# Performance work log

Hardware: AMD Instinct MI355X
Metric: run time of the kernel (lower is better)

The kernel has to match this reference:

```python
import jax, jax.numpy as jnp
import numpy as np
import math

D = 128      # out_dim (= d)
H = 4        # n_heads
DK = D // H  # d_k = 32
M = 5        # fixed num types in forward
NN = 15      # fixed N in forward
SQRT_DK = math.sqrt(DK)


def setup_inputs() -> dict:
    key = jax.random.key(0)
    ks = jax.random.split(key, 18)
    b, n = 1024, 64
    inp = {
        "node_inp": jax.random.normal(ks[0], (D, b, n), jnp.float32),
        "WW": jax.random.normal(ks[1], (b, M, n, NN), jnp.float32) * 0.1,
        "mask_matrix": jax.random.uniform(ks[2], (M * NN, n), jnp.float32),
        "R": jax.random.normal(ks[3], (b, H, n, n), jnp.float32),
        "attn_mask": jax.random.uniform(ks[4], (1, 1, n, 4 * n), jnp.float32),
        # learned parameters (xavier-ish scale)
        "WK": jax.random.normal(ks[5], (M, D, D), jnp.float32) * 0.05,
        "bK": jax.random.normal(ks[6], (M, D, 1), jnp.float32) * 0.05,
        "WQ": jax.random.normal(ks[7], (M, D, D), jnp.float32) * 0.05,
        "bQ": jax.random.normal(ks[8], (M, D, 1), jnp.float32) * 0.05,
        "WM": jax.random.normal(ks[9], (M, D, D), jnp.float32) * 0.05,
        "bM": jax.random.normal(ks[10], (M, D, 1), jnp.float32) * 0.05,
        "WB": jax.random.normal(ks[11], (M, D, D), jnp.float32) * 0.05,
        "bB": jax.random.normal(ks[12], (M, D, 1), jnp.float32) * 0.05,
        "Wmsgup": jax.random.normal(ks[13], (DK, DK), jnp.float32) * 0.1,
        "Wmsgdown": jax.random.normal(ks[14], (DK, DK), jnp.float32) * 0.1,
        "Wmsgleft": jax.random.normal(ks[15], (DK, DK), jnp.float32) * 0.1,
        "Wmsgright": jax.random.normal(ks[16], (DK, DK), jnp.float32) * 0.1,
    }
    return inp


def reference(node_inp, WW, mask_matrix, R, attn_mask,
              WK, bK, WQ, bQ, WM, bM, WB, bB,
              Wmsgup, Wmsgdown, Wmsgleft, Wmsgright):
    d, b, n = node_inp.shape
    # project node features through per-type mixing: (b, m, d, N)
    node_inp_m = jnp.einsum('dbn,bmnN->bmdN', node_inp, WW)

    def proj_perm(W, bias):
        # per-type linear then permute(0,2,1,3) before flatten (as K/Q do)
        x = jnp.einsum('mde,bmeN->bmdN', W, node_inp_m) + bias[None]  # (b,m,d,N)
        x = x.transpose(0, 2, 1, 3).reshape(b, d, M * NN)
        return x @ mask_matrix  # (b, d, n)

    K = proj_perm(WK, bK).reshape(b, H, DK, n)
    Q = proj_perm(WQ, bQ).reshape(b, H, DK, n)

    # message: NOTE original reshapes (b*m,d,N) -> (b,d,m*N) WITHOUT the permute; replicate faithfully
    msg = jnp.einsum('mde,bmeN->bmdN', WM, node_inp_m) + bM[None]  # (b,m,d,N)
    message = msg.reshape(b, d, M * NN) @ mask_matrix               # (b, d, n)

    A = jnp.einsum('bhki,bhkj->bhij', Q, K) / SQRT_DK               # (b,h,n,n)
    aw = jax.nn.softmax(R + A, axis=3)
    aw = jnp.where(jnp.isnan(aw), jnp.zeros_like(aw), aw)
    aw = jnp.tile(aw, (1, 1, 1, 4)) * attn_mask                     # (b,h,n,4n)

    res_msg = message.reshape(b, H, DK, n)
    Wmsg = jnp.concatenate([Wmsgup, Wmsgdown, Wmsgleft, Wmsgright], axis=1)  # (dk, 4dk)
    res = jnp.einsum('kq,bhkn->bhqn', Wmsg, res_msg)                # (b,h,4dk,n)
    res = res.reshape(b, H, DK, 4 * n)                               # faithful reshape

    B = jnp.einsum('bhnm,bhkm->bhkn', aw, res).reshape(b, d, n)
    B = jax.nn.gelu(B, approximate=False)

    Bm = jnp.einsum('bdn,bmnN->bmdN', B, WW)
    Bm = jnp.einsum('mde,bmeN->bmdN', WB, Bm) + bB[None]
    Bm = Bm.transpose(0, 2, 1, 3).reshape(b, d, M * NN) @ mask_matrix  # (b,d,n)
    out = Bm.transpose(1, 0, 2) + node_inp                             # (d,b,n)
    return (out, aw[0, 0])
```

## Files before the change

kernel.cpp:

```cpp
#include <hip/hip_runtime.h>
#include <math.h>

#define Dd 128
#define Hh 4
#define DKk 32
#define Mm 5
#define NNn 15
#define Bb 1024
#define Nn 64
#define MN 75
#define BN 65536
#define RSQRT_DK 0.17677669529663687f

typedef __attribute__((ext_vector_type(8))) short bf16x8;
typedef __attribute__((ext_vector_type(4))) float f32x4;

__device__ __forceinline__ ushort f2bf(float x) {
    unsigned u = __float_as_uint(x);
    u = (u + 0x7fffu + ((u >> 16) & 1u)) >> 16;
    return (ushort)u;
}
__device__ __forceinline__ float bf2f(ushort h) {
    return __uint_as_float(((unsigned)h) << 16);
}
__device__ __forceinline__ void split2(float x, ushort& hi, ushort& lo) {
    hi = f2bf(x);
    lo = f2bf(x - bf2f(hi));
}
__device__ __forceinline__ f32x4 MFMA(bf16x8 a, bf16x8 b, f32x4 c) {
    return __builtin_amdgcn_mfma_f32_16x16x32_bf16(a, b, c, 0, 0, 0);
}

__global__ void k0_prep(const float* __restrict__ maskm,
                        const float* __restrict__ WK, const float* __restrict__ bK,
                        const float* __restrict__ WQ, const float* __restrict__ bQ,
                        const float* __restrict__ WM, const float* __restrict__ bM,
                        const float* __restrict__ WB, const float* __restrict__ bB,
                        const float* __restrict__ Wu, const float* __restrict__ Wd,
                        const float* __restrict__ Wl, const float* __restrict__ Wr,
                        ushort* __restrict__ WKhi, ushort* __restrict__ WKlo,
                        ushort* __restrict__ WQhi, ushort* __restrict__ WQlo,
                        ushort* __restrict__ WMhi, ushort* __restrict__ WBhi,
                        ushort* __restrict__ maskhi, ushort* __restrict__ masklo,
                        ushort* __restrict__ maskThi, ushort* __restrict__ maskTlo,
                        float* __restrict__ btK, float* __restrict__ btQ,
                        float* __restrict__ btM, float* __restrict__ btB,
                        ushort* __restrict__ WcatT)
{
    int tid = blockIdx.x * blockDim.x + threadIdx.x;
    int nthr = gridDim.x * blockDim.x;
    const int NW = Mm * Dd * Dd;
    for (int i = tid; i < NW; i += nthr) {
        split2(WK[i], WKhi[i], WKlo[i]);
        split2(WQ[i], WQhi[i], WQlo[i]);
        WMhi[i] = f2bf(WM[i]);
        WBhi[i] = f2bf(WB[i]);
    }
    for (int i = tid; i < 96 * 64; i += nthr) {
        float v = (i < MN * 64) ? maskm[i] : 0.f;
        split2(v, maskhi[i], masklo[i]);
    }
    for (int i = tid; i < 64 * 96; i += nthr) {
        int col = i / 96, j = i - col * 96;
        float v = (j < MN) ? maskm[j * 64 + col] : 0.f;
        split2(v, maskThi[i], maskTlo[i]);
    }
    for (int i = tid; i < 4096; i += nthr) {
        int q = i >> 5, kk = i & 31;
        const float* Wsel = (q < 32) ? Wu : (q < 64) ? Wd : (q < 96) ? Wl : Wr;
        WcatT[i] = f2bf(Wsel[kk * 32 + (q & 31)]);
    }
    for (int i = tid; i < 8192; i += nthr) {
        int d = i >> 6, col = i & 63;
        float aKv = 0.f, aQv = 0.f, aBv = 0.f;
        for (int m = 0; m < Mm; ++m) {
            float mrs = 0.f;
            for (int N = 0; N < NNn; ++N) mrs += maskm[(m * 15 + N) * 64 + col];
            aKv += bK[m * 128 + d] * mrs;
            aQv += bQ[m * 128 + d] * mrs;
            aBv += bB[m * 128 + d] * mrs;
        }
        btK[i] = aKv; btQ[i] = aQv; btB[i] = aBv;
        float aMv = 0.f;
        int dd = d;
        for (int j = 0; j < MN; ++j) {
            int f = dd * 75 + j;
            int m = f / 1920;
            int dloc = (f / 15) & 127;
            aMv += bM[m * 128 + dloc] * maskm[j * 64 + col];
        }
        btM[i] = aMv;
    }
}

__global__ __launch_bounds__(512, 4) void k1_proj(
    const float* __restrict__ node, const float* __restrict__ WW,
    const ushort* __restrict__ WKhi, const ushort* __restrict__ WKlo,
    const ushort* __restrict__ WQhi, const ushort* __restrict__ WQlo,
    const ushort* __restrict__ WMhi,
    const ushort* __restrict__ maskThi, const ushort* __restrict__ maskTlo,
    const float* __restrict__ btK, const float* __restrict__ btQ,
    const float* __restrict__ btM,
    float* __restrict__ Kout, float* __restrict__ Qout, ushort* __restrict__ msgB)
{
    const int b = blockIdx.x;
    const int tid = threadIdx.x;
    const int lane = tid & 63, w = tid >> 6;
    const int l15 = lane & 15, lq = lane >> 4;

    __shared__ ushort nimTh[80 * 136];
    __shared__ ushort nimTl[80 * 136];
    __shared__ ushort planes[4 * 32 * 104];

    ushort* Ykh = planes;
    ushort* Ykl = planes + 32 * 104;
    ushort* Yqh = planes + 2 * 32 * 104;
    ushort* Yql = planes + 3 * 32 * 104;

    for (int t = tid; t < 5 * 136; t += 512) {
        int mm = t / 136, e = t - mm * 136;
        nimTh[(mm * 16 + 15) * 136 + e] = 0;
        nimTl[(mm * 16 + 15) * 136 + e] = 0;
    }
    for (int t = tid; t < 128 * 29; t += 512) {
        int r = t / 29, cc = 75 + (t - r * 29);
        planes[r * 104 + cc] = 0;
    }

    const f32x4 zz = {0.f, 0.f, 0.f, 0.f};

    {
        bf16x8 ah[2], al[2];
        #pragma unroll
        for (int ks = 0; ks < 2; ++ks) {
            const float* np = node + (size_t)(w * 16 + l15) * BN + b * 64 + ks * 32 + lq * 8;
            float tmp[8];
            *(float4*)tmp       = *(const float4*)np;
            *(float4*)(tmp + 4) = *(const float4*)(np + 4);
            #pragma unroll
            for (int j = 0; j < 8; ++j) {
                ushort h_, l_; split2(tmp[j], h_, l_);
                ah[ks][j] = (short)h_; al[ks][j] = (short)l_;
            }
        }
        for (int m = 0; m < Mm; ++m) {
            const float* wp = WW + ((size_t)b * Mm + m) * 960 + (l15 < 15 ? l15 : 0);
            f32x4 c = zz;
            #pragma unroll
            for (int ks = 0; ks < 2; ++ks) {
                bf16x8 bh, bl;
                #pragma unroll
                for (int t = 0; t < 8; ++t) {
                    int n = ks * 32 + lq * 8 + t;
                    float v = (l15 < 15) ? wp[n * 15] : 0.f;
                    ushort h_, l_; split2(v, h_, l_);
                    bh[t] = (short)h_; bl[t] = (short)l_;
                }
                c = MFMA(ah[ks], bh, c); c = MFMA(ah[ks], bl, c); c = MFMA(al[ks], bh, c);
            }
            if (l15 < 15) {
                #pragma unroll
                for (int t = 0; t < 4; ++t) {
                    int e = w * 16 + lq * 4 + t;
                    split2(c[t], nimTh[(m * 16 + l15) * 136 + e],
                                 nimTl[(m * 16 + l15) * 136 + e]);
                }
            }
        }
    }
    __syncthreads();

    for (int qd = 0; qd < 4; ++qd) {
        for (int u = w; u < 10; u += 8) {
            int m = u >> 1, rt = u & 1;
            int d0 = qd * 32 + rt * 16 + l15;
            f32x4 cK = zz, cQ = zz;
            #pragma unroll
            for (int ks = 0; ks < 4; ++ks) {
                int k0 = ks * 32 + lq * 8;
                size_t wo = (size_t)m * 16384 + (size_t)d0 * 128 + k0;
                bf16x8 kh = *(const bf16x8*)(WKhi + wo);
                bf16x8 kl = *(const bf16x8*)(WKlo + wo);
                bf16x8 qh = *(const bf16x8*)(WQhi + wo);
                bf16x8 ql = *(const bf16x8*)(WQlo + wo);
                bf16x8 bh = *(const bf16x8*)(&nimTh[(m * 16 + l15) * 136 + k0]);
                bf16x8 bl = *(const bf16x8*)(&nimTl[(m * 16 + l15) * 136 + k0]);
                cK = MFMA(kh, bh, cK); cK = MFMA(kh, bl, cK); cK = MFMA(kl, bh, cK);
                cQ = MFMA(qh, bh, cQ); cQ = MFMA(qh, bl, cQ); cQ = MFMA(ql, bh, cQ);
            }
            if (l15 < 15) {
                int j = m * 15 + l15;
                #pragma unroll
                for (int t = 0; t < 4; ++t) {
                    int r = rt * 16 + lq * 4 + t;
                    split2(cK[t], Ykh[r * 104 + j], Ykl[r * 104 + j]);
                    split2(cQ[t], Yqh[r * 104 + j], Yql[r * 104 + j]);
                }
            }
        }
        __syncthreads();
        {
            int rt = w >> 2, ct = w & 3;
            bf16x8 mh[3], ml[3];
            #pragma unroll
            for (int ks = 0; ks < 3; ++ks) {
                int k0 = ks * 32 + lq * 8;
                mh[ks] = *(const bf16x8*)(maskThi + (ct * 16 + l15) * 96 + k0);
                ml[ks] = *(const bf16x8*)(maskTlo + (ct * 16 + l15) * 96 + k0);
            }
            f32x4 cK = zz, cQ = zz;
            #pragma unroll
            for (int ks = 0; ks < 3; ++ks) {
                int k0 = ks * 32 + lq * 8;
                bf16x8 ah = *(const bf16x8*)(&Ykh[(rt * 16 + l15) * 104 + k0]);
                bf16x8 al = *(const bf16x8*)(&Ykl[(rt * 16 + l15) * 104 + k0]);
                cK = MFMA(ah, mh[ks], cK); cK = MFMA(ah, ml[ks], cK); cK = MFMA(al, mh[ks], cK);
                bf16x8 qa = *(const bf16x8*)(&Yqh[(rt * 16 + l15) * 104 + k0]);
                bf16x8 qb = *(const bf16x8*)(&Yql[(rt * 16 + l15) * 104 + k0]);
                cQ = MFMA(qa, mh[ks], cQ); cQ = MFMA(qa, ml[ks], cQ); cQ = MFMA(qb, mh[ks], cQ);
            }
            #pragma unroll
            for (int t = 0; t < 4; ++t) {
                int d = qd * 32 + rt * 16 + lq * 4 + t;
                int col = ct * 16 + l15;
                size_t gi = (size_t)b * 8192 + (size_t)d * 64 + col;
                Kout[gi] = cK[t] + btK[d * 64 + col];
                Qout[gi] = cQ[t] + btQ[d * 64 + col];
            }
        }
        __syncthreads();
    }

    {
        int rt = w;
        for (int m = 0; m < Mm; ++m) {
            f32x4 c = zz;
            #pragma unroll
            for (int ks = 0; ks < 4; ++ks) {
                int k0 = ks * 32 + lq * 8;
                bf16x8 a  = *(const bf16x8*)(WMhi + (size_t)m * 16384 + (size_t)(rt * 16 + l15) * 128 + k0);
                bf16x8 bh = *(const bf16x8*)(&nimTh[(m * 16 + l15) * 136 + k0]);
                c = MFMA(a, bh, c);
            }
            if (l15 < 15) {
                #pragma unroll
                for (int t = 0; t < 4; ++t) {
                    int d = rt * 16 + lq * 4 + t;
                    int g = m * 1920 + d * 15 + l15;
                    planes[(g / 75) * 104 + (g % 75)] = f2bf(c[t]);
                }
            }
        }
    }
    __syncthreads();
    #pragma unroll
    for (int s = 0; s < 4; ++s) {
        int u = w * 4 + s;
        int rt = u & 7, ct = u >> 3;
        f32x4 c = zz;
        #pragma unroll
        for (int ks = 0; ks < 3; ++ks) {
            int k0 = ks * 32 + lq * 8;
            bf16x8 a  = *(const bf16x8*)(&planes[(rt * 16 + l15) * 104 + k0]);
            bf16x8 bh = *(const bf16x8*)(maskThi + (ct * 16 + l15) * 96 + k0);
            c = MFMA(a, bh, c);
        }
        #pragma unroll
        for (int t = 0; t < 4; ++t) {
            int dd = rt * 16 + lq * 4 + t;
            int col = ct * 16 + l15;
            msgB[(size_t)b * 8192 + dd * 64 + col] = f2bf(c[t] + btM[dd * 64 + col]);
        }
    }
}

__global__ __launch_bounds__(512, 4) void k2_attn(
    const float* __restrict__ Kd, const float* __restrict__ Qd,
    ushort* msgB,
    const float* __restrict__ R, const float* __restrict__ am,
    const ushort* __restrict__ WcatT, float* __restrict__ aw00)
{
    const int b = blockIdx.x >> 2, h = blockIdx.x & 3;
    const int tid = threadIdx.x;
    const int lane = tid & 63, w = tid >> 6;
    const int l15 = lane & 15, lq = lane >> 4;

    __shared__ ushort QTh[64 * 40], QTl[64 * 40];
    __shared__ ushort KTh[64 * 40], KTl[64 * 40];
    __shared__ ushort msgT[64 * 40];
    __shared__ float  ST[64 * 65];
    __shared__ ushort resS[128 * 72];
    __shared__ ushort awq[64 * 72];

    const size_t base = (size_t)b * 8192 + h * 2048;
    for (int i = tid; i < 2048; i += 512) {
        int d = i >> 6, n = i & 63;
        ushort hi, lo;
        split2(Qd[base + i], hi, lo); QTh[n * 40 + d] = hi; QTl[n * 40 + d] = lo;
        split2(Kd[base + i], hi, lo); KTh[n * 40 + d] = hi; KTl[n * 40 + d] = lo;
        msgT[n * 40 + d] = msgB[base + i];
    }
    __syncthreads();

    const float* Rb = R + ((size_t)b * Hh + h) * 4096;
    {
        int ti = w >> 1;
        bf16x8 ah = *reinterpret_cast<const bf16x8*>(&QTh[(ti * 16 + l15) * 40 + lq * 8]);
        bf16x8 al = *reinterpret_cast<const bf16x8*>(&QTl[(ti * 16 + l15) * 40 + lq * 8]);
        #pragma unroll
        for (int s = 0; s < 2; ++s) {
            int tj = (w & 1) * 2 + s;
            bf16x8 bh = *reinterpret_cast<const bf16x8*>(&KTh[(tj * 16 + l15) * 40 + lq * 8]);
            bf16x8 bl = *reinterpret_cast<const bf16x8*>(&KTl[(tj * 16 + l15) * 40 + lq * 8]);
            f32x4 c = {0.f, 0.f, 0.f, 0.f};
            c = MFMA(ah, bh, c); c = MFMA(ah, bl, c); c = MFMA(al, bh, c);
            #pragma unroll
            for (int r = 0; r < 4; ++r) {
                int i = ti * 16 + lq * 4 + r, j = tj * 16 + l15;
                ST[j * 65 + i] = Rb[i * 64 + j] + c[r] * RSQRT_DK;
            }
        }
    }
    {
        bf16x8 a = *reinterpret_cast<const bf16x8*>(WcatT + (w * 16 + l15) * 32 + lq * 8);
        #pragma unroll
        for (int nt = 0; nt < 4; ++nt) {
            bf16x8 bfr = *reinterpret_cast<const bf16x8*>(&msgT[(nt * 16 + l15) * 40 + lq * 8]);
            f32x4 c = {0.f, 0.f, 0.f, 0.f};
            c = MFMA(a, bfr, c);
            #pragma unroll
            for (int r = 0; r < 4; ++r)
                resS[(w * 16 + lq * 4 + r) * 72 + nt * 16 + l15] = f2bf(c[r]);
        }
    }
    __syncthreads();

    {
        int row = tid >> 3, part = tid & 7;
        float v[8]; float mx = -INFINITY;
        #pragma unroll
        for (int jj = 0; jj < 8; ++jj) { v[jj] = ST[(part * 8 + jj) * 65 + row]; mx = fmaxf(mx, v[jj]); }
        mx = fmaxf(mx, __shfl_xor(mx, 1));
        mx = fmaxf(mx, __shfl_xor(mx, 2));
        mx = fmaxf(mx, __shfl_xor(mx, 4));
        float s = 0.f;
        #pragma unroll
        for (int jj = 0; jj < 8; ++jj) { v[jj] = expf(v[jj] - mx); s += v[jj]; }
        s += __shfl_xor(s, 1); s += __shfl_xor(s, 2); s += __shfl_xor(s, 4);
        float inv = 1.f / s;
        #pragma unroll
        for (int jj = 0; jj < 8; ++jj) {
            float p = v[jj] * inv;
            ST[(part * 8 + jj) * 65 + row] = isnan(p) ? 0.f : p;
        }
    }
    __syncthreads();

    const int kt = w >> 2, it = w & 3;
    f32x4 accB = {0.f, 0.f, 0.f, 0.f};
    for (int q = 0; q < 4; ++q) {
        for (int e = tid; e < 4096; e += 512) {
            int i = e >> 6, j0 = e & 63;
            float p = ST[j0 * 65 + i] * am[i * 256 + q * 64 + j0];
            awq[i * 72 + j0] = f2bf(p);
            if (blockIdx.x == 0) aw00[i * 256 + q * 64 + j0] = p;
        }
        __syncthreads();
        #pragma unroll
        for (int ks = 0; ks < 2; ++ks) {
            int row = 4 * (kt * 16 + l15) + q;
            bf16x8 a   = *reinterpret_cast<const bf16x8*>(&resS[row * 72 + ks * 32 + lq * 8]);
            bf16x8 bfr = *reinterpret_cast<const bf16x8*>(&awq[(it * 16 + l15) * 72 + ks * 32 + lq * 8]);
            accB = MFMA(a, bfr, accB);
        }
        __syncthreads();
    }

    #pragma unroll
    for (int r = 0; r < 4; ++r) {
        int k = kt * 16 + lq * 4 + r, i = it * 16 + l15;
        float x = accB[r];
        float g = 0.5f * x * (1.f + erff(x * 0.70710678118654752f));
        msgB[base + k * 64 + i] = f2bf(g);
    }
}

__global__ __launch_bounds__(512, 4) void k3_out(
    const ushort* __restrict__ Bbuf, const float* __restrict__ WW,
    const ushort* __restrict__ WBhi, const ushort* __restrict__ maskhi,
    const float* __restrict__ btB, const float* __restrict__ node,
    float* __restrict__ outp)
{
    const int b = blockIdx.x, tid = threadIdx.x;
    const int lane = tid & 63, w = tid >> 6, l15 = lane & 15, lq = lane >> 4;
    __shared__ ushort sB[128 * 66];
    __shared__ ushort wwh[64 * 17];
    __shared__ ushort t1[128 * 17];
    __shared__ ushort nm[32 * 66];

    for (int i = tid; i < 8192; i += 512) {
        int d = i >> 6, n = i & 63;
        sB[d * 66 + n] = Bbuf[(size_t)b * 8192 + i];
    }
    const f32x4 zz = {0.f, 0.f, 0.f, 0.f};
    f32x4 acc[4];
    for (int c = 0; c < 4; ++c) acc[c] = zz;
    __syncthreads();

    for (int m = 0; m < Mm; ++m) {
        for (int i = tid; i < 64 * 17; i += 512) {
            int n = i / 17, N = i - n * 17;
            wwh[i] = (N < 15) ? f2bf(WW[(((size_t)b * Mm + m) * 64 + n) * 15 + N]) : (ushort)0;
        }
        __syncthreads();
        {
            f32x4 c = zz;
            for (int ks = 0; ks < 2; ++ks) {
                int k0 = ks * 32 + (lq << 3);
                bf16x8 a, bh;
                #pragma unroll
                for (int t = 0; t < 8; ++t) {
                    a[t] = (short)sB[(w * 16 + l15) * 66 + k0 + t];
                    bh[t] = (short)wwh[(k0 + t) * 17 + l15];
                }
                c = MFMA(a, bh, c);
            }
            #pragma unroll
            for (int t = 0; t < 4; ++t)
                t1[(w * 16 + lq * 4 + t) * 17 + l15] = f2bf(c[t]);
        }
        __syncthreads();

        bf16x8 mfh;
        {
            int ct = w & 3;
            int k0 = lq << 3;
            #pragma unroll
            for (int t = 0; t < 8; ++t) {
                int kk = k0 + t;
                int row = (kk < 15) ? (m * 15 + kk) : 95;
                mfh[t] = (short)maskhi[row * 64 + ct * 16 + l15];
            }
        }
        for (int eb = 0; eb < 4; ++eb) {
            {
                int rtl = w >> 2, ct = w & 3;
                int e = eb * 32 + rtl * 16 + l15;
                int k0 = lq << 3;
                bf16x8 a;
                #pragma unroll
                for (int t = 0; t < 8; ++t) {
                    int kk = k0 + t;
                    int cc = (kk < 15) ? kk : 15;
                    a[t] = (short)t1[e * 17 + cc];
                }
                f32x4 c = zz;
                c = MFMA(a, mfh, c);
                #pragma unroll
                for (int t = 0; t < 4; ++t)
                    nm[(rtl * 16 + lq * 4 + t) * 66 + ct * 16 + l15] = f2bf(c[t]);
            }
            __syncthreads();
            {
                size_t aoff = (size_t)(w * 16 + l15) * 128 + eb * 32 + (lq << 3);
                bf16x8 a = *reinterpret_cast<const bf16x8*>(WBhi + m * 16384 + aoff);
                int k0 = lq << 3;
                #pragma unroll
                for (int ct = 0; ct < 4; ++ct) {
                    bf16x8 bh;
                    #pragma unroll
                    for (int t = 0; t < 8; ++t) bh[t] = (short)nm[(k0 + t) * 66 + ct * 16 + l15];
                    acc[ct] = MFMA(a, bh, acc[ct]);
                }
            }
            __syncthreads();
        }
    }
    #pragma unroll
    for (int ct = 0; ct < 4; ++ct) {
        #pragma unroll
        for (int t = 0; t < 4; ++t) {
            int d = w * 16 + lq * 4 + t;
            int col = ct * 16 + l15;
            size_t gi = (size_t)d * BN + b * 64 + col;
            outp[gi] = acc[ct][t] + btB[d * 64 + col] + node[gi];
        }
    }
}

extern "C" void kernel_launch(void* const* d_in, const int* in_sizes, int n_in,
                              void* d_out, int out_size, void* d_ws, size_t ws_size,
                              hipStream_t stream) {
    const float* node  = (const float*)d_in[0];
    const float* WW    = (const float*)d_in[1];
    const float* maskm = (const float*)d_in[2];
    const float* R     = (const float*)d_in[3];
    const float* am    = (const float*)d_in[4];
    const float* WK = (const float*)d_in[5];  const float* bK = (const float*)d_in[6];
    const float* WQ = (const float*)d_in[7];  const float* bQ = (const float*)d_in[8];
    const float* WM = (const float*)d_in[9];  const float* bM = (const float*)d_in[10];
    const float* WB = (const float*)d_in[11]; const float* bB = (const float*)d_in[12];
    const float* Wu = (const float*)d_in[13]; const float* Wd = (const float*)d_in[14];
    const float* Wl = (const float*)d_in[15]; const float* Wr = (const float*)d_in[16];

    float* out  = (float*)d_out;
    float* aw00 = out + (size_t)Dd * BN;

    char* W = (char*)d_ws;
    float*  Qbuf   = (float*)W;
    ushort* msgB   = (ushort*)(W + 33554432);
    ushort* WKhi   = (ushort*)(W + 50331648);
    ushort* WKlo   = WKhi + 81920;
    ushort* WQhi   = WKlo + 81920;
    ushort* WQlo   = WQhi + 81920;
    ushort* WMhi   = WQlo + 81920;
    ushort* WBhi   = WMhi + 81920;
    ushort* maskhi = WBhi + 81920;
    ushort* masklo = maskhi + 6144;
    float*  btK    = (float*)(masklo + 6144);
    float*  btQ    = btK + 8192;
    float*  btM    = btQ + 8192;
    float*  btB    = btM + 8192;
    ushort* WcatT  = (ushort*)(btB + 8192);
    ushort* maskThi = WcatT + 4096;
    ushort* maskTlo = maskThi + 6144;

    k0_prep<<<512, 256, 0, stream>>>(maskm, WK, bK, WQ, bQ, WM, bM, WB, bB,
                                     Wu, Wd, Wl, Wr,
                                     WKhi, WKlo, WQhi, WQlo, WMhi, WBhi,
                                     maskhi, masklo, maskThi, maskTlo,
                                     btK, btQ, btM, btB, WcatT);
    k1_proj<<<Bb, 512, 0, stream>>>(node, WW, WKhi, WKlo, WQhi, WQlo, WMhi,
                                    maskThi, maskTlo, btK, btQ, btM,
                                    out, Qbuf, msgB);
    k2_attn<<<Bb * Hh, 512, 0, stream>>>(out, Qbuf, msgB, R, am, WcatT, aw00);
    k3_out<<<Bb, 512, 0, stream>>>(msgB, WW, WBhi, maskhi, btB, node, out);
}
```

Baseline: 297.4 us.

## Emit pre-split, head-transposed bf16 K/Q/msg from projection; drop attention LDS staging

The projection kernel now writes K and Q as bf16 hi/lo planes and the message as bf16, all laid out per (batch, head) as [n][dk]. The attention kernel can then load MFMA fragments straight from global memory, which removes its fp32 load, split and LDS transpose staging and one barrier. MFMA chains are also split into independent accumulators that are summed at the end, to expose more instruction-level parallelism. The output kernel now reads B with vectorized LDS loads. The GELU output of attention is written into the Q-hi buffer, reusing memory that block has already consumed, and the output buffer serves as scratch for K.

New measurement: 279.7 us. 1.06x faster.

```diff
diff --git a/kernel.cpp b/kernel.cpp
--- a/kernel.cpp
+++ b/kernel.cpp
@@ -43,8 +43,8 @@
                         ushort* __restrict__ WMhi, ushort* __restrict__ WBhi,
                         ushort* __restrict__ maskhi, ushort* __restrict__ masklo,
                         ushort* __restrict__ maskThi, ushort* __restrict__ maskTlo,
-                        float* __restrict__ btK, float* __restrict__ btQ,
-                        float* __restrict__ btM, float* __restrict__ btB,
+                        float* __restrict__ btKT, float* __restrict__ btQT,
+                        float* __restrict__ btMT, float* __restrict__ btB,
                         ushort* __restrict__ WcatT)
 {
     int tid = blockIdx.x * blockDim.x + threadIdx.x;
@@ -80,16 +80,17 @@
             aQv += bQ[m * 128 + d] * mrs;
             aBv += bB[m * 128 + d] * mrs;
         }
-        btK[i] = aKv; btQ[i] = aQv; btB[i] = aBv;
+        btKT[col * 128 + d] = aKv;
+        btQT[col * 128 + d] = aQv;
+        btB[i] = aBv;
         float aMv = 0.f;
-        int dd = d;
         for (int j = 0; j < MN; ++j) {
-            int f = dd * 75 + j;
+            int f = d * 75 + j;
             int m = f / 1920;
             int dloc = (f / 15) & 127;
             aMv += bM[m * 128 + dloc] * maskm[j * 64 + col];
         }
-        btM[i] = aMv;
+        btMT[col * 128 + d] = aMv;
     }
 }
 
@@ -99,9 +100,11 @@
     const ushort* __restrict__ WQhi, const ushort* __restrict__ WQlo,
     const ushort* __restrict__ WMhi,
     const ushort* __restrict__ maskThi, const ushort* __restrict__ maskTlo,
-    const float* __restrict__ btK, const float* __restrict__ btQ,
-    const float* __restrict__ btM,
-    float* __restrict__ Kout, float* __restrict__ Qout, ushort* __restrict__ msgB)
+    const float* __restrict__ btKT, const float* __restrict__ btQT,
+    const float* __restrict__ btMT,
+    ushort* __restrict__ Khi, ushort* __restrict__ Klo,
+    ushort* __restrict__ Qhi, ushort* __restrict__ Qlo,
+    ushort* __restrict__ msgTg)
 {
     const int b = blockIdx.x;
     const int tid = threadIdx.x;
@@ -145,7 +148,7 @@
         }
         for (int m = 0; m < Mm; ++m) {
             const float* wp = WW + ((size_t)b * Mm + m) * 960 + (l15 < 15 ? l15 : 0);
-            f32x4 c = zz;
+            f32x4 chh = zz, chl = zz, clh = zz;
             #pragma unroll
             for (int ks = 0; ks < 2; ++ks) {
                 bf16x8 bh, bl;
@@ -156,8 +159,11 @@
                     ushort h_, l_; split2(v, h_, l_);
                     bh[t] = (short)h_; bl[t] = (short)l_;
                 }
-                c = MFMA(ah[ks], bh, c); c = MFMA(ah[ks], bl, c); c = MFMA(al[ks], bh, c);
-            }
+                chh = MFMA(ah[ks], bh, chh);
+                chl = MFMA(ah[ks], bl, chl);
+                clh = MFMA(al[ks], bh, clh);
+            }
+            f32x4 c = chh + chl + clh;
             if (l15 < 15) {
                 #pragma unroll
                 for (int t = 0; t < 4; ++t) {
@@ -174,20 +180,23 @@
         for (int u = w; u < 10; u += 8) {
             int m = u >> 1, rt = u & 1;
             int d0 = qd * 32 + rt * 16 + l15;
-            f32x4 cK = zz, cQ = zz;
+            f32x4 khh = zz, khl = zz, klh = zz;
+            f32x4 qhh = zz, qhl = zz, qlh = zz;
             #pragma unroll
             for (int ks = 0; ks < 4; ++ks) {
                 int k0 = ks * 32 + lq * 8;
                 size_t wo = (size_t)m * 16384 + (size_t)d0 * 128 + k0;
-                bf16x8 kh = *(const bf16x8*)(WKhi + wo);
-                bf16x8 kl = *(const bf16x8*)(WKlo + wo);
-                bf16x8 qh = *(const bf16x8*)(WQhi + wo);
-                bf16x8 ql = *(const bf16x8*)(WQlo + wo);
+                bf16x8 akh = *(const bf16x8*)(WKhi + wo);
+                bf16x8 akl = *(const bf16x8*)(WKlo + wo);
+                bf16x8 aqh = *(const bf16x8*)(WQhi + wo);
+                bf16x8 aql = *(const bf16x8*)(WQlo + wo);
                 bf16x8 bh = *(const bf16x8*)(&nimTh[(m * 16 + l15) * 136 + k0]);
                 bf16x8 bl = *(const bf16x8*)(&nimTl[(m * 16 + l15) * 136 + k0]);
-                cK = MFMA(kh, bh, cK); cK = MFMA(kh, bl, cK); cK = MFMA(kl, bh, cK);
-                cQ = MFMA(qh, bh, cQ); cQ = MFMA(qh, bl, cQ); cQ = MFMA(ql, bh, cQ);
-            }
+                khh = MFMA(akh, bh, khh); khl = MFMA(akh, bl, khl); klh = MFMA(akl, bh, klh);
+                qhh = MFMA(aqh, bh, qhh); qhl = MFMA(aqh, bl, qhl); qlh = MFMA(aql, bh, qlh);
+            }
+            f32x4 cK = khh + khl + klh;
+            f32x4 cQ = qhh + qhl + qlh;
             if (l15 < 15) {
                 int j = m * 15 + l15;
                 #pragma unroll
@@ -200,32 +209,34 @@
         }
         __syncthreads();
         {
-            int rt = w >> 2, ct = w & 3;
-            bf16x8 mh[3], ml[3];
+            int nr = w & 3, dc = w >> 2;
+            f32x4 khh = zz, khl = zz, klh = zz;
+            f32x4 qhh = zz, qhl = zz, qlh = zz;
             #pragma unroll
             for (int ks = 0; ks < 3; ++ks) {
                 int k0 = ks * 32 + lq * 8;
-                mh[ks] = *(const bf16x8*)(maskThi + (ct * 16 + l15) * 96 + k0);
-                ml[ks] = *(const bf16x8*)(maskTlo + (ct * 16 + l15) * 96 + k0);
-            }
-            f32x4 cK = zz, cQ = zz;
-            #pragma unroll
-            for (int ks = 0; ks < 3; ++ks) {
-                int k0 = ks * 32 + lq * 8;
-                bf16x8 ah = *(const bf16x8*)(&Ykh[(rt * 16 + l15) * 104 + k0]);
-                bf16x8 al = *(const bf16x8*)(&Ykl[(rt * 16 + l15) * 104 + k0]);
-                cK = MFMA(ah, mh[ks], cK); cK = MFMA(ah, ml[ks], cK); cK = MFMA(al, mh[ks], cK);
-                bf16x8 qa = *(const bf16x8*)(&Yqh[(rt * 16 + l15) * 104 + k0]);
-                bf16x8 qb = *(const bf16x8*)(&Yql[(rt * 16 + l15) * 104 + k0]);
-                cQ = MFMA(qa, mh[ks], cQ); cQ = MFMA(qa, ml[ks], cQ); cQ = MFMA(qb, mh[ks], cQ);
-            }
+                bf16x8 mh = *(const bf16x8*)(maskThi + (nr * 16 + l15) * 96 + k0);
+                bf16x8 ml = *(const bf16x8*)(maskTlo + (nr * 16 + l15) * 96 + k0);
+                bf16x8 ykh = *(const bf16x8*)(&Ykh[(dc * 16 + l15) * 104 + k0]);
+                bf16x8 ykl = *(const bf16x8*)(&Ykl[(dc * 16 + l15) * 104 + k0]);
+                bf16x8 yqh = *(const bf16x8*)(&Yqh[(dc * 16 + l15) * 104 + k0]);
+                bf16x8 yql = *(const bf16x8*)(&Yql[(dc * 16 + l15) * 104 + k0]);
+                khh = MFMA(mh, ykh, khh); khl = MFMA(ml, ykh, khl); klh = MFMA(mh, ykl, klh);
+                qhh = MFMA(mh, yqh, qhh); qhl = MFMA(ml, yqh, qhl); qlh = MFMA(mh, yql, qlh);
+            }
+            f32x4 cK = khh + khl + klh;
+            f32x4 cQ = qhh + qhl + qlh;
             #pragma unroll
             for (int t = 0; t < 4; ++t) {
-                int d = qd * 32 + rt * 16 + lq * 4 + t;
-                int col = ct * 16 + l15;
-                size_t gi = (size_t)b * 8192 + (size_t)d * 64 + col;
-                Kout[gi] = cK[t] + btK[d * 64 + col];
-                Qout[gi] = cQ[t] + btQ[d * 64 + col];
+                int n = nr * 16 + lq * 4 + t;
+                int dloc = dc * 16 + l15;
+                int d = qd * 32 + dloc;
+                size_t oi = (((size_t)(b * 4 + qd)) * 64 + n) * 32 + dloc;
+                ushort hh_, ll_;
+                split2(cK[t] + btKT[n * 128 + d], hh_, ll_);
+                Khi[oi] = hh_; Klo[oi] = ll_;
+                split2(cQ[t] + btQT[n * 128 + d], hh_, ll_);
+                Qhi[oi] = hh_; Qlo[oi] = ll_;
             }
         }
         __syncthreads();
@@ -234,19 +245,20 @@
     {
         int rt = w;
         for (int m = 0; m < Mm; ++m) {
-            f32x4 c = zz;
+            f32x4 c0 = zz, c1 = zz;
             #pragma unroll
             for (int ks = 0; ks < 4; ++ks) {
                 int k0 = ks * 32 + lq * 8;
                 bf16x8 a  = *(const bf16x8*)(WMhi + (size_t)m * 16384 + (size_t)(rt * 16 + l15) * 128 + k0);
                 bf16x8 bh = *(const bf16x8*)(&nimTh[(m * 16 + l15) * 136 + k0]);
-                c = MFMA(a, bh, c);
-            }
+                if (ks < 2) c0 = MFMA(a, bh, c0); else c1 = MFMA(a, bh, c1);
+            }
+            f32x4 c = c0 + c1;
             if (l15 < 15) {
                 #pragma unroll
                 for (int t = 0; t < 4; ++t) {
-                    int d = rt * 16 + lq * 4 + t;
-                    int g = m * 1920 + d * 15 + l15;
+                    int dflat = rt * 16 + lq * 4 + t;
+                    int g = m * 1920 + dflat * 15 + l15;
                     planes[(g / 75) * 104 + (g % 75)] = f2bf(c[t]);
                 }
             }
@@ -256,64 +268,63 @@
     #pragma unroll
     for (int s = 0; s < 4; ++s) {
         int u = w * 4 + s;
-        int rt = u & 7, ct = u >> 3;
-        f32x4 c = zz;
-        #pragma unroll
-        for (int ks = 0; ks < 3; ++ks) {
-            int k0 = ks * 32 + lq * 8;
-            bf16x8 a  = *(const bf16x8*)(&planes[(rt * 16 + l15) * 104 + k0]);
-            bf16x8 bh = *(const bf16x8*)(maskThi + (ct * 16 + l15) * 96 + k0);
-            c = MFMA(a, bh, c);
-        }
+        int nr = u & 3, ddc = u >> 2;
+        f32x4 cs0 = zz, cs1 = zz, cs2 = zz;
+        {
+            bf16x8 a0 = *(const bf16x8*)(maskThi + (nr * 16 + l15) * 96 + lq * 8);
+            bf16x8 b0 = *(const bf16x8*)(&planes[(ddc * 16 + l15) * 104 + lq * 8]);
+            cs0 = MFMA(a0, b0, cs0);
+            bf16x8 a1 = *(const bf16x8*)(maskThi + (nr * 16 + l15) * 96 + 32 + lq * 8);
+            bf16x8 b1 = *(const bf16x8*)(&planes[(ddc * 16 + l15) * 104 + 32 + lq * 8]);
+            cs1 = MFMA(a1, b1, cs1);
+            bf16x8 a2 = *(const bf16x8*)(maskThi + (nr * 16 + l15) * 96 + 64 + lq * 8);
+            bf16x8 b2 = *(const bf16x8*)(&planes[(ddc * 16 + l15) * 104 + 64 + lq * 8]);
+            cs2 = MFMA(a2, b2, cs2);
+        }
+        f32x4 c = cs0 + cs1 + cs2;
         #pragma unroll
         for (int t = 0; t < 4; ++t) {
-            int dd = rt * 16 + lq * 4 + t;
-            int col = ct * 16 + l15;
-            msgB[(size_t)b * 8192 + dd * 64 + col] = f2bf(c[t] + btM[dd * 64 + col]);
+            int n = nr * 16 + lq * 4 + t;
+            int dd = ddc * 16 + l15;
+            int h = dd >> 5, dk = dd & 31;
+            msgTg[(((size_t)(b * 4 + h)) * 64 + n) * 32 + dk] = f2bf(c[t] + btMT[n * 128 + dd]);
         }
     }
 }
 
 __global__ __launch_bounds__(512, 4) void k2_attn(
-    const float* __restrict__ Kd, const float* __restrict__ Qd,
-    ushort* msgB,
+    const ushort* __restrict__ Khi, const ushort* __restrict__ Klo,
+    const ushort* Qhi, const ushort* __restrict__ Qlo,
+    const ushort* __restrict__ msgTg,
     const float* __restrict__ R, const float* __restrict__ am,
-    const ushort* __restrict__ WcatT, float* __restrict__ aw00)
+    const ushort* __restrict__ WcatT, float* __restrict__ aw00,
+    ushort* Bout)
 {
     const int b = blockIdx.x >> 2, h = blockIdx.x & 3;
     const int tid = threadIdx.x;
     const int lane = tid & 63, w = tid >> 6;
     const int l15 = lane & 15, lq = lane >> 4;
 
-    __shared__ ushort QTh[64 * 40], QTl[64 * 40];
-    __shared__ ushort KTh[64 * 40], KTl[64 * 40];
-    __shared__ ushort msgT[64 * 40];
     __shared__ float  ST[64 * 65];
     __shared__ ushort resS[128 * 72];
     __shared__ ushort awq[64 * 72];
 
-    const size_t base = (size_t)b * 8192 + h * 2048;
-    for (int i = tid; i < 2048; i += 512) {
-        int d = i >> 6, n = i & 63;
-        ushort hi, lo;
-        split2(Qd[base + i], hi, lo); QTh[n * 40 + d] = hi; QTl[n * 40 + d] = lo;
-        split2(Kd[base + i], hi, lo); KTh[n * 40 + d] = hi; KTl[n * 40 + d] = lo;
-        msgT[n * 40 + d] = msgB[base + i];
-    }
-    __syncthreads();
-
-    const float* Rb = R + ((size_t)b * Hh + h) * 4096;
+    const f32x4 zz = {0.f, 0.f, 0.f, 0.f};
+    const size_t base2 = (size_t)(b * 4 + h) * 2048;
+    const float* Rb = R + (size_t)(b * 4 + h) * 4096;
+
     {
         int ti = w >> 1;
-        bf16x8 ah = *reinterpret_cast<const bf16x8*>(&QTh[(ti * 16 + l15) * 40 + lq * 8]);
-        bf16x8 al = *reinterpret_cast<const bf16x8*>(&QTl[(ti * 16 + l15) * 40 + lq * 8]);
+        bf16x8 ah = *(const bf16x8*)(Qhi + base2 + (size_t)(ti * 16 + l15) * 32 + lq * 8);
+        bf16x8 al = *(const bf16x8*)(Qlo + base2 + (size_t)(ti * 16 + l15) * 32 + lq * 8);
         #pragma unroll
         for (int s = 0; s < 2; ++s) {
             int tj = (w & 1) * 2 + s;
-            bf16x8 bh = *reinterpret_cast<const bf16x8*>(&KTh[(tj * 16 + l15) * 40 + lq * 8]);
-            bf16x8 bl = *reinterpret_cast<const bf16x8*>(&KTl[(tj * 16 + l15) * 40 + lq * 8]);
-            f32x4 c = {0.f, 0.f, 0.f, 0.f};
-            c = MFMA(ah, bh, c); c = MFMA(ah, bl, c); c = MFMA(al, bh, c);
+            bf16x8 bh = *(const bf16x8*)(Khi + base2 + (size_t)(tj * 16 + l15) * 32 + lq * 8);
+            bf16x8 bl = *(const bf16x8*)(Klo + base2 + (size_t)(tj * 16 + l15) * 32 + lq * 8);
+            f32x4 chh = zz, chl = zz, clh = zz;
+            chh = MFMA(ah, bh, chh); chl = MFMA(ah, bl, chl); clh = MFMA(al, bh, clh);
+            f32x4 c = chh + chl + clh;
             #pragma unroll
             for (int r = 0; r < 4; ++r) {
                 int i = ti * 16 + lq * 4 + r, j = tj * 16 + l15;
@@ -322,12 +333,11 @@
         }
     }
     {
-        bf16x8 a = *reinterpret_cast<const bf16x8*>(WcatT + (w * 16 + l15) * 32 + lq * 8);
+        bf16x8 a = *(const bf16x8*)(WcatT + (w * 16 + l15) * 32 + lq * 8);
         #pragma unroll
         for (int nt = 0; nt < 4; ++nt) {
-            bf16x8 bfr = *reinterpret_cast<const bf16x8*>(&msgT[(nt * 16 + l15) * 40 + lq * 8]);
-            f32x4 c = {0.f, 0.f, 0.f, 0.f};
-            c = MFMA(a, bfr, c);
+            bf16x8 bfr = *(const bf16x8*)(msgTg + base2 + (size_t)(nt * 16 + l15) * 32 + lq * 8);
+            f32x4 c = MFMA(a, bfr, zz);
             #pragma unroll
             for (int r = 0; r < 4; ++r)
                 resS[(w * 16 + lq * 4 + r) * 72 + nt * 16 + l15] = f2bf(c[r]);
@@ -357,7 +367,7 @@
     __syncthreads();
 
     const int kt = w >> 2, it = w & 3;
-    f32x4 accB = {0.f, 0.f, 0.f, 0.f};
+    f32x4 accB0 = zz, accB1 = zz;
     for (int q = 0; q < 4; ++q) {
         for (int e = tid; e < 4096; e += 512) {
             int i = e >> 6, j0 = e & 63;
@@ -366,41 +376,42 @@
             if (blockIdx.x == 0) aw00[i * 256 + q * 64 + j0] = p;
         }
         __syncthreads();
-        #pragma unroll
-        for (int ks = 0; ks < 2; ++ks) {
-            int row = 4 * (kt * 16 + l15) + q;
-            bf16x8 a   = *reinterpret_cast<const bf16x8*>(&resS[row * 72 + ks * 32 + lq * 8]);
-            bf16x8 bfr = *reinterpret_cast<const bf16x8*>(&awq[(it * 16 + l15) * 72 + ks * 32 + lq * 8]);
-            accB = MFMA(a, bfr, accB);
-        }
+        int row = 4 * (kt * 16 + l15) + q;
+        bf16x8 a0 = *(const bf16x8*)(&resS[row * 72 + lq * 8]);
+        bf16x8 b0 = *(const bf16x8*)(&awq[(it * 16 + l15) * 72 + lq * 8]);
+        accB0 = MFMA(a0, b0, accB0);
+        bf16x8 a1 = *(const bf16x8*)(&resS[row * 72 + 32 + lq * 8]);
+        bf16x8 b1 = *(const bf16x8*)(&awq[(it * 16 + l15) * 72 + 32 + lq * 8]);
+        accB1 = MFMA(a1, b1, accB1);
         __syncthreads();
     }
+    f32x4 accB = accB0 + accB1;
 
     #pragma unroll
     for (int r = 0; r < 4; ++r) {
         int k = kt * 16 + lq * 4 + r, i = it * 16 + l15;
         float x = accB[r];
         float g = 0.5f * x * (1.f + erff(x * 0.70710678118654752f));
-        msgB[base + k * 64 + i] = f2bf(g);
+        Bout[base2 + k * 64 + i] = f2bf(g);
     }
 }
 
 __global__ __launch_bounds__(512, 4) void k3_out(
-    const ushort* __restrict__ Bbuf, const float* __restrict__ WW,
+    const ushort* Bbuf, const float* __restrict__ WW,
     const ushort* __restrict__ WBhi, const ushort* __restrict__ maskhi,
     const float* __restrict__ btB, const float* __restrict__ node,
     float* __restrict__ outp)
 {
     const int b = blockIdx.x, tid = threadIdx.x;
     const int lane = tid & 63, w = tid >> 6, l15 = lane & 15, lq = lane >> 4;
-    __shared__ ushort sB[128 * 66];
+    __shared__ ushort sB[128 * 72];
     __shared__ ushort wwh[64 * 17];
     __shared__ ushort t1[128 * 17];
     __shared__ ushort nm[32 * 66];
 
     for (int i = tid; i < 8192; i += 512) {
         int d = i >> 6, n = i & 63;
-        sB[d * 66 + n] = Bbuf[(size_t)b * 8192 + i];
+        sB[d * 72 + n] = Bbuf[(size_t)b * 8192 + i];
     }
     const f32x4 zz = {0.f, 0.f, 0.f, 0.f};
     f32x4 acc[4];
@@ -414,17 +425,17 @@
         }
         __syncthreads();
         {
-            f32x4 c = zz;
+            f32x4 c0 = zz, c1 = zz;
+            #pragma unroll
             for (int ks = 0; ks < 2; ++ks) {
                 int k0 = ks * 32 + (lq << 3);
-                bf16x8 a, bh;
-                #pragma unroll
-                for (int t = 0; t < 8; ++t) {
-                    a[t] = (short)sB[(w * 16 + l15) * 66 + k0 + t];
-                    bh[t] = (short)wwh[(k0 + t) * 17 + l15];
-                }
-                c = MFMA(a, bh, c);
-            }
+                bf16x8 a = *(const bf16x8*)(&sB[(w * 16 + l15) * 72 + k0]);
+                bf16x8 bh;
+                #pragma unroll
+                for (int t = 0; t < 8; ++t) bh[t] = (short)wwh[(k0 + t) * 17 + l15];
+                if (ks == 0) c0 = MFMA(a, bh, c0); else c1 = MFMA(a, bh, c1);
+            }
+            f32x4 c = c0 + c1;
             #pragma unroll
             for (int t = 0; t < 4; ++t)
                 t1[(w * 16 + lq * 4 + t) * 17 + l15] = f2bf(c[t]);
@@ -463,7 +474,7 @@
             __syncthreads();
             {
                 size_t aoff = (size_t)(w * 16 + l15) * 128 + eb * 32 + (lq << 3);
-                bf16x8 a = *reinterpret_cast<const bf16x8*>(WBhi + m * 16384 + aoff);
+                bf16x8 a = *(const bf16x8*)(WBhi + m * 16384 + aoff);
                 int k0 = lq << 3;
                 #pragma unroll
                 for (int ct = 0; ct < 4; ++ct) {
@@ -506,33 +517,38 @@
     float* out  = (float*)d_out;
     float* aw00 = out + (size_t)Dd * BN;
 
+    ushort* Khi = (ushort*)d_out;
+    ushort* Klo = Khi + 8388608;
+
     char* W = (char*)d_ws;
-    float*  Qbuf   = (float*)W;
-    ushort* msgB   = (ushort*)(W + 33554432);
-    ushort* WKhi   = (ushort*)(W + 50331648);
-    ushort* WKlo   = WKhi + 81920;
-    ushort* WQhi   = WKlo + 81920;
-    ushort* WQlo   = WQhi + 81920;
-    ushort* WMhi   = WQlo + 81920;
-    ushort* WBhi   = WMhi + 81920;
-    ushort* maskhi = WBhi + 81920;
-    ushort* masklo = maskhi + 6144;
-    float*  btK    = (float*)(masklo + 6144);
-    float*  btQ    = btK + 8192;
-    float*  btM    = btQ + 8192;
-    float*  btB    = btM + 8192;
-    ushort* WcatT  = (ushort*)(btB + 8192);
-    ushort* maskThi = WcatT + 4096;
+    ushort* Qhi   = (ushort*)W;
+    ushort* Qlo   = Qhi + 8388608;
+    ushort* msgTg = Qlo + 8388608;
+    ushort* WKhi  = msgTg + 8388608;
+    ushort* WKlo  = WKhi + 81920;
+    ushort* WQhi  = WKlo + 81920;
+    ushort* WQlo  = WQhi + 81920;
+    ushort* WMhi  = WQlo + 81920;
+    ushort* WBhi  = WMhi + 81920;
+    ushort* maskhi  = WBhi + 81920;
+    ushort* masklo  = maskhi + 6144;
+    ushort* maskThi = masklo + 6144;
     ushort* maskTlo = maskThi + 6144;
+    ushort* WcatT   = maskTlo + 6144;
+    float*  btKT = (float*)(WcatT + 4096);
+    float*  btQT = btKT + 8192;
+    float*  btMT = btQT + 8192;
+    float*  btB  = btMT + 8192;
 
     k0_prep<<<512, 256, 0, stream>>>(maskm, WK, bK, WQ, bQ, WM, bM, WB, bB,
                                      Wu, Wd, Wl, Wr,
                                      WKhi, WKlo, WQhi, WQlo, WMhi, WBhi,
                                      maskhi, masklo, maskThi, maskTlo,
-                                     btK, btQ, btM, btB, WcatT);
+                                     btKT, btQT, btMT, btB, WcatT);
     k1_proj<<<Bb, 512, 0, stream>>>(node, WW, WKhi, WKlo, WQhi, WQlo, WMhi,
-                                    maskThi, maskTlo, btK, btQ, btM,
-                                    out, Qbuf, msgB);
-    k2_attn<<<Bb * Hh, 512, 0, stream>>>(out, Qbuf, msgB, R, am, WcatT, aw00);
-    k3_out<<<Bb, 512, 0, stream>>>(msgB, WW, WBhi, maskhi, btB, node, out);
-}
+                                    maskThi, maskTlo, btKT, btQT, btMT,
+                                    Khi, Klo, Qhi, Qlo, msgTg);
+    k2_attn<<<Bb * Hh, 512, 0, stream>>>(Khi, Klo, Qhi, Qlo, msgTg, R, am,
+                                         WcatT, aw00, Qhi );
+    k3_out<<<Bb, 512, 0, stream>>>(Qhi , WW, WBhi, maskhi, btB, node, out);
+}
```
